# Kernel optimization log

Measured on AMD Instinct MI355X. Metric: run time of the kernel, lower is better.

Reference implementation:

```python
import jax, jax.numpy as jnp
import numpy as np

B, N, DM = 4, 4096, 768
H, LH = 12, 4          # total heads, local heads
GH = H - LH            # global (FAVOR+) heads
DH = DM // H           # 64, head dim
M = 256                # nb random features
W = 128                # local window size
EPS = 1e-4


def _gaussian_orthogonal_matrix(m, d, rng):
    # performer-pytorch gaussian_orthogonal_random_matrix, scaling=0
    blocks = []
    for _ in range(int(np.ceil(m / d))):
        q, _ = np.linalg.qr(rng.standard_normal((d, d)))
        blocks.append(q.T)
    mat = np.concatenate(blocks, 0)[:m]
    multiplier = np.linalg.norm(rng.standard_normal((m, d)), axis=-1)
    return (multiplier[:, None] * mat).astype(np.float32)


def setup_inputs() -> dict:
    key = jax.random.key(0)
    ks = jax.random.split(key, 6)
    s = 0.02
    x = jax.random.normal(ks[0], (B, N, DM), jnp.float32)
    mask = jnp.ones((B, N), dtype=bool)
    Wq = jax.random.normal(ks[1], (DM, DM), jnp.float32) * s
    Wk = jax.random.normal(ks[2], (DM, DM), jnp.float32) * s
    Wv = jax.random.normal(ks[3], (DM, DM), jnp.float32) * s
    Wo = jax.random.normal(ks[4], (DM, DM), jnp.float32) * s
    bo = jnp.zeros((DM,), jnp.float32)
    proj = jnp.asarray(_gaussian_orthogonal_matrix(M, DH, np.random.default_rng(0)))
    return {"x": x, "mask": mask, "Wq": Wq, "Wk": Wk, "Wv": Wv,
            "Wo": Wo, "bo": bo, "proj": proj}


def _softmax_kernel(data, proj, is_query):
    # FAVOR+ positive random features for the softmax kernel
    d = data.shape[-1]
    normalizer = d ** -0.25
    ratio = proj.shape[0] ** -0.5
    dd = jnp.einsum('bhnd,md->bhnm', data * normalizer, proj)
    diag = jnp.sum(data ** 2, axis=-1) * 0.5 * (normalizer ** 2)  # (b,h,n)
    if is_query:
        stab = jnp.max(dd, axis=-1, keepdims=True)
        return ratio * (jnp.exp(dd - diag[..., None] - stab) + EPS)
    stab = jnp.max(dd)
    return ratio * (jnp.exp(dd - diag[..., None] - stab) + EPS)


def _favor_attention(q, k, v, proj):
    # non-causal linear attention: O(n * m * d)
    qp = _softmax_kernel(q, proj, True)    # (b,gh,n,m)
    kp = _softmax_kernel(k, proj, False)   # (b,gh,n,m)
    k_sum = kp.sum(axis=2)                               # (b,gh,m)
    d_inv = 1.0 / jnp.einsum('bhnm,bhm->bhn', qp, k_sum)
    context = jnp.einsum('bhnm,bhnd->bhmd', kp, v)       # (b,gh,m,d)
    return jnp.einsum('bhmd,bhnm,bhn->bhnd', context, qp, d_inv)


def _rotary(x):
    # SinusoidalEmbeddings + apply_rotary_pos_emb (NeoX half-rotation)
    n, d = x.shape[-2], x.shape[-1]
    half = d // 2
    inv_freq = 1.0 / (10000.0 ** (jnp.arange(0, d, 2, dtype=jnp.float32) / d))
    freqs = jnp.arange(n, dtype=jnp.float32)[:, None] * inv_freq[None, :]
    emb = jnp.concatenate([freqs, freqs], axis=-1)       # (n,d)
    cos, sin = jnp.cos(emb), jnp.sin(emb)
    x1, x2 = x[..., :half], x[..., half:]
    rot = jnp.concatenate([-x2, x1], axis=-1)
    return x * cos + rot * sin


def _local_attention(lq, lk, lv, mask):
    # windowed attention, look_backward=1, look_forward=1 (non-causal)
    b, h, n, d = lq.shape
    lq, lk = _rotary(lq), _rotary(lk)
    nw = n // W
    bq = lq.reshape(b, h, nw, W, d)
    bk = lk.reshape(b, h, nw, W, d)
    bv = lv.reshape(b, h, nw, W, d)

    def look5(t):  # gather previous/current/next window along window axis
        p = jnp.pad(t, ((0, 0), (0, 0), (1, 1), (0, 0), (0, 0)))
        return jnp.concatenate([p[:, :, i:i + nw] for i in range(3)], axis=3)

    bk, bv = look5(bk), look5(bv)                        # (b,h,nw,3W,d)
    dots = jnp.einsum('bhwie,bhwje->bhwij', bq, bk) * (d ** -0.5)

    ticker = jnp.arange(n).reshape(nw, W)
    tp = jnp.pad(ticker, ((1, 1), (0, 0)), constant_values=-1)
    bq_k = jnp.concatenate([tp[i:i + nw] for i in range(3)], axis=1)  # (nw,3W)
    pad_ok = (bq_k != -1)[None, None, :, None, :]

    mq = mask.reshape(b, nw, W)
    mkp = jnp.pad(mq, ((0, 0), (1, 1), (0, 0)), constant_values=False)
    mk = jnp.concatenate([mkp[:, i:i + nw] for i in range(3)], axis=2)  # (b,nw,3W)
    inp_ok = (mq[:, :, :, None] & mk[:, :, None, :])[:, None]          # (b,1,nw,W,3W)

    neg = -jnp.finfo(dots.dtype).max
    dots = jnp.where(pad_ok & inp_ok, dots, neg)
    attn = jax.nn.softmax(dots, axis=-1)
    out = jnp.einsum('bhwij,bhwje->bhwie', attn, bv)
    return out.reshape(b, h, n, d)


def reference(x, mask, Wq, Wk, Wv, Wo, bo, proj):
    b, n, _ = x.shape
    split = lambda t: t.reshape(b, n, H, DH).transpose(0, 2, 1, 3)  # (b,h,n,d)
    q, k, v = split(x @ Wq), split(x @ Wk), split(x @ Wv)
    qg, lq = q[:, :GH], q[:, GH:]
    kg, lk = k[:, :GH], k[:, GH:]
    vg, lv = v[:, :GH], v[:, GH:]
    # global heads: zero masked values, FAVOR+ linear attention
    vg = jnp.where(mask[:, None, :, None], vg, 0.0)
    out_g = _favor_attention(qg, kg, vg, proj)
    out_l = _local_attention(lq, lk, lv, mask)
    out = jnp.concatenate([out_g, out_l], axis=1)        # (b,H,n,d)
    out = out.transpose(0, 2, 1, 3).reshape(b, n, DM)
    return out @ Wo + bo
```

## Files before the change

kernel.cpp:

```cpp
#include <hip/hip_runtime.h>
#include <hip/hip_fp16.h>
#include <math.h>

#define BB 4
#define NN 4096
#define DMM 768
#define HHH 12
#define LHH 4
#define GHH 8
#define DH 64
#define MM 256
#define WW 128
#define NWIN (NN/WW)
#define EPSF 1.0e-4f
#define NRM 0.35355339059327373f
#define NRM2 0.125f
#define RATIO 0.0625f
#define LN1E4_32 0.28782313662425572f

using bf16x8 = __attribute__((ext_vector_type(8))) short;
using fp16x8 = __attribute__((ext_vector_type(8))) _Float16;
using f32x4  = __attribute__((ext_vector_type(4))) float;

static __device__ __forceinline__ unsigned enc_f32(float f) {
  unsigned u = __float_as_uint(f);
  return (u & 0x80000000u) ? ~u : (u | 0x80000000u);
}
static __device__ __forceinline__ float dec_f32(unsigned u) {
  unsigned b = (u & 0x80000000u) ? (u ^ 0x80000000u) : ~u;
  return __uint_as_float(b);
}
static __device__ __forceinline__ unsigned short f2h(float x) {
  return __half_as_ushort(__float2half(x));
}
static __device__ __forceinline__ void gload16(const unsigned short* g, unsigned short* l) {
  __builtin_amdgcn_global_load_lds(
      (const __attribute__((address_space(1))) void*)g,
      (__attribute__((address_space(3))) void*)l, 16, 0, 0);
}

__global__ __launch_bounds__(256) void w_split(
    const float* __restrict__ W, unsigned short* __restrict__ Whi)
{
  int o = blockIdx.x * 256 + threadIdx.x;
  int k = o / DMM, n = o % DMM;
  Whi[(size_t)n * DMM + k] = f2h(W[o]);
}

__global__ __launch_bounds__(256) void a_split(
    const float* __restrict__ A, unsigned short* __restrict__ Ahi,
    unsigned short* __restrict__ Alo)
{
  size_t o = ((size_t)blockIdx.x * 256 + threadIdx.x) * 4;
  float4 v = *(const float4*)(A + o);
  float f[4] = {v.x, v.y, v.z, v.w};
  unsigned short hi[4], lo[4];
#pragma unroll
  for (int i = 0; i < 4; ++i) {
    __half h = __float2half(f[i]);
    hi[i] = __half_as_ushort(h);
    lo[i] = f2h(f[i] - __half2float(h));
  }
  *(uint2*)(Ahi + o) = *(uint2*)&hi[0];
  *(uint2*)(Alo + o) = *(uint2*)&lo[0];
}

__global__ __launch_bounds__(256) void gemm_mfma(
    const float* __restrict__ A, const unsigned short* __restrict__ Bhi,
    const float* __restrict__ bias, float* __restrict__ C, int K, int Nc)
{
  __shared__ unsigned short Ah[128][40];
  __shared__ unsigned short Al[128][40];
  __shared__ unsigned short Bh[128][40];

  const int tid = threadIdx.x;
  const int wid = tid >> 6, lane = tid & 63;
  const int quad = lane >> 4, l16 = lane & 15;
  const int row0 = blockIdx.y * 128;
  const int col0 = blockIdx.x * 128;
  const int wm = (wid & 1) * 64, wn = (wid >> 1) * 64;
  const int sr = tid >> 1;
  const int sk = (tid & 1) * 16;

  f32x4 acc[4][4];
  const f32x4 zf = {0.f, 0.f, 0.f, 0.f};
#pragma unroll
  for (int i = 0; i < 4; ++i)
#pragma unroll
    for (int j = 0; j < 4; ++j) acc[i][j] = zf;

  for (int k0 = 0; k0 < K; k0 += 32) {
    __syncthreads();
    {
      const float* a = A + (size_t)(row0 + sr) * K + k0 + sk;
      float fv[16];
      *(float4*)&fv[0]  = *(const float4*)(a);
      *(float4*)&fv[4]  = *(const float4*)(a + 4);
      *(float4*)&fv[8]  = *(const float4*)(a + 8);
      *(float4*)&fv[12] = *(const float4*)(a + 12);
      unsigned hw[8], lw[8];
#pragma unroll
      for (int p = 0; p < 8; ++p) {
        float x0 = fv[2 * p], x1 = fv[2 * p + 1];
        __half h0 = __float2half(x0), h1 = __float2half(x1);
        unsigned short l0 = f2h(x0 - __half2float(h0));
        unsigned short l1 = f2h(x1 - __half2float(h1));
        hw[p] = (unsigned)__half_as_ushort(h0) | ((unsigned)__half_as_ushort(h1) << 16);
        lw[p] = (unsigned)l0 | ((unsigned)l1 << 16);
      }
      *(uint4*)&Ah[sr][sk]     = *(uint4*)&hw[0];
      *(uint4*)&Ah[sr][sk + 8] = *(uint4*)&hw[4];
      *(uint4*)&Al[sr][sk]     = *(uint4*)&lw[0];
      *(uint4*)&Al[sr][sk + 8] = *(uint4*)&lw[4];
    }
    {
      const unsigned short* bh = Bhi + (size_t)(col0 + sr) * DMM + k0 + sk;
      *(uint4*)&Bh[sr][sk]     = *(const uint4*)(bh);
      *(uint4*)&Bh[sr][sk + 8] = *(const uint4*)(bh + 8);
    }
    __syncthreads();

    fp16x8 afh[4], afl[4], bfh[4];
#pragma unroll
    for (int t = 0; t < 4; ++t) {
      afh[t] = *(const fp16x8*)&Ah[wm + t * 16 + l16][quad * 8];
      afl[t] = *(const fp16x8*)&Al[wm + t * 16 + l16][quad * 8];
      bfh[t] = *(const fp16x8*)&Bh[wn + t * 16 + l16][quad * 8];
    }
#pragma unroll
    for (int ti = 0; ti < 4; ++ti)
#pragma unroll
      for (int tj = 0; tj < 4; ++tj) {
        acc[ti][tj] = __builtin_amdgcn_mfma_f32_16x16x32_f16(afh[ti], bfh[tj], acc[ti][tj], 0, 0, 0);
        acc[ti][tj] = __builtin_amdgcn_mfma_f32_16x16x32_f16(afl[ti], bfh[tj], acc[ti][tj], 0, 0, 0);
      }
  }

  float bv[4] = {0.f, 0.f, 0.f, 0.f};
  if (bias) {
#pragma unroll
    for (int tj = 0; tj < 4; ++tj) bv[tj] = bias[col0 + wn + tj * 16 + l16];
  }
#pragma unroll
  for (int ti = 0; ti < 4; ++ti) {
    const int gr = row0 + wm + ti * 16 + quad * 4;
#pragma unroll
    for (int tj = 0; tj < 4; ++tj) {
      const int gc = col0 + wn + tj * 16 + l16;
      float* cp = C + (size_t)gr * Nc + gc;
#pragma unroll
      for (int r = 0; r < 4; ++r)
        cp[(size_t)r * Nc] = acc[ti][tj][r] + bv[tj];
    }
  }
}

__global__ __launch_bounds__(256) void gemm_mfma_pre(
    const unsigned short* __restrict__ Ahi, const unsigned short* __restrict__ Alo,
    const unsigned short* __restrict__ Bhi,
    const float* __restrict__ bias, float* __restrict__ C, int K, int Nc)
{
  __shared__ unsigned short Ah[128][32];
  __shared__ unsigned short Al[128][32];
  __shared__ unsigned short Bh[128][32];

  const int tid = threadIdx.x;
  const int wid = tid >> 6, lane = tid & 63;
  const int quad = lane >> 4, l16 = lane & 15;

  const int nwg = gridDim.x * gridDim.y;
  int hw = blockIdx.y * gridDim.x + blockIdx.x;
  int logical = ((nwg & 7) == 0) ? ((hw & 7) * (nwg >> 3) + (hw >> 3)) : hw;
  const int col0 = (logical % gridDim.x) * 128;
  const int row0 = (logical / gridDim.x) * 128;

  const int wm = (wid & 1) * 64, wn = (wid >> 1) * 64;
  const int sw8 = (quad ^ ((l16 >> 1) & 3)) * 8;

  const int rr = tid >> 2;
  const int cg8 = ((tid & 3) ^ ((tid >> 3) & 3)) * 8;

  f32x4 acc[4][4];
  const f32x4 zf = {0.f, 0.f, 0.f, 0.f};
#pragma unroll
  for (int i = 0; i < 4; ++i)
#pragma unroll
    for (int j = 0; j < 4; ++j) acc[i][j] = zf;

  for (int k0 = 0; k0 < K; k0 += 32) {
    __syncthreads();
    {
      const size_t ro0 = (size_t)(row0 + rr) * K + k0 + cg8;
      const size_t ro1 = (size_t)(row0 + 64 + rr) * K + k0 + cg8;
      const size_t co0 = (size_t)(col0 + rr) * K + k0 + cg8;
      const size_t co1 = (size_t)(col0 + 64 + rr) * K + k0 + cg8;
      unsigned short* la  = &Ah[0][0] + tid * 8;
      unsigned short* lal = &Al[0][0] + tid * 8;
      unsigned short* lb  = &Bh[0][0] + tid * 8;
      gload16(Ahi + ro0, la);
      gload16(Ahi + ro1, la + 2048);
      gload16(Alo + ro0, lal);
      gload16(Alo + ro1, lal + 2048);
      gload16(Bhi + co0, lb);
      gload16(Bhi + co1, lb + 2048);
    }
    __syncthreads();

    fp16x8 afh[4], afl[4], bfh[4];
#pragma unroll
    for (int t = 0; t < 4; ++t) {
      afh[t] = *(const fp16x8*)&Ah[wm + t * 16 + l16][sw8];
      afl[t] = *(const fp16x8*)&Al[wm + t * 16 + l16][sw8];
      bfh[t] = *(const fp16x8*)&Bh[wn + t * 16 + l16][sw8];
    }
#pragma unroll
    for (int ti = 0; ti < 4; ++ti)
#pragma unroll
      for (int tj = 0; tj < 4; ++tj) {
        acc[ti][tj] = __builtin_amdgcn_mfma_f32_16x16x32_f16(afh[ti], bfh[tj], acc[ti][tj], 0, 0, 0);
        acc[ti][tj] = __builtin_amdgcn_mfma_f32_16x16x32_f16(afl[ti], bfh[tj], acc[ti][tj], 0, 0, 0);
      }
  }

  float bv[4] = {0.f, 0.f, 0.f, 0.f};
  if (bias) {
#pragma unroll
    for (int tj = 0; tj < 4; ++tj) bv[tj] = bias[col0 + wn + tj * 16 + l16];
  }
#pragma unroll
  for (int ti = 0; ti < 4; ++ti) {
    const int gr = row0 + wm + ti * 16 + quad * 4;
#pragma unroll
    for (int tj = 0; tj < 4; ++tj) {
      const int gc = col0 + wn + tj * 16 + l16;
      float* cp = C + (size_t)gr * Nc + gc;
#pragma unroll
      for (int r = 0; r < 4; ++r)
        cp[(size_t)r * Nc] = acc[ti][tj][r] + bv[tj];
    }
  }
}

__global__ void init_stab(unsigned* stab_enc) {
  if (threadIdx.x == 0 && blockIdx.x == 0) *stab_enc = 0x00800000u;
}

__global__ __launch_bounds__(256) void transpose_proj(
    const float* __restrict__ proj, float* __restrict__ projT,
    unsigned short* __restrict__ phh, unsigned short* __restrict__ phl)
{
  int o = blockIdx.x * 256 + threadIdx.x;
  int k = o >> 8, m = o & 255;
  float v = proj[m * 64 + k];
  projT[k * 256 + m] = v;
  __half hh = __float2half(v);
  float lf = v - __half2float(hh);
  phh[m * 64 + k] = __half_as_ushort(hh);
  phl[m * 64 + k] = f2h(lf);
}

__global__ __launch_bounds__(256) void rot_qk(
    const float* __restrict__ Qb, const float* __restrict__ Kb,
    unsigned short* __restrict__ Qlh, unsigned short* __restrict__ Klh)
{
  int idx = blockIdx.x * 256 + threadIdx.x;
  int n = idx & (NN - 1);
  int bh = idx >> 12;
  int b = bh >> 2, h = bh & 3;
  const float* qs = Qb + ((size_t)(b * NN + n)) * DMM + GHH * DH + h * DH;
  const float* ks = Kb + ((size_t)(b * NN + n)) * DMM + GHH * DH + h * DH;
  float q[64], k[64];
#pragma unroll
  for (int t = 0; t < 16; ++t) {
    *(float4*)&q[t * 4] = *(const float4*)(qs + t * 4);
    *(float4*)&k[t * 4] = *(const float4*)(ks + t * 4);
  }
  unsigned short qo[64], ko[64];
#pragma unroll
  for (int i = 0; i < 32; ++i) {
    float invf = __expf((float)i * -LN1E4_32);
    float th = (float)n * invf;
    float s, c;
    sincosf(th, &s, &c);
    qo[i]      = f2h(fmaf(q[i], c, -q[i + 32] * s) * NRM2);
    qo[i + 32] = f2h(fmaf(q[i + 32], c, q[i] * s) * NRM2);
    ko[i]      = f2h(fmaf(k[i], c, -k[i + 32] * s));
    ko[i + 32] = f2h(fmaf(k[i + 32], c, k[i] * s));
  }
  unsigned short* qd = Qlh + (size_t)idx * 64;
  unsigned short* kd = Klh + (size_t)idx * 64;
#pragma unroll
  for (int t = 0; t < 8; ++t) {
    *(uint4*)(qd + t * 8) = *(uint4*)&qo[t * 8];
    *(uint4*)(kd + t * 8) = *(uint4*)&ko[t * 8];
  }
}

__global__ __launch_bounds__(256) void v_trans(
    const float* __restrict__ Vb, unsigned short* __restrict__ Vt)
{
  __shared__ unsigned short T[64][72];
  const int nb = blockIdx.x, h = blockIdx.y, b = blockIdx.z;
  const int n0 = nb * 64;
  const int tid = threadIdx.x;
  {
    int r = tid >> 2, g = tid & 3;
    const float* src = Vb + ((size_t)(b * NN + n0 + r)) * DMM + GHH * DH + h * DH + g * 16;
#pragma unroll
    for (int t = 0; t < 4; ++t) {
      float4 v = *(const float4*)(src + t * 4);
      T[g * 16 + t * 4 + 0][r] = f2h(v.x);
      T[g * 16 + t * 4 + 1][r] = f2h(v.y);
      T[g * 16 + t * 4 + 2][r] = f2h(v.z);
      T[g * 16 + t * 4 + 3][r] = f2h(v.w);
    }
  }
  __syncthreads();
  {
    int d = tid >> 2, g = tid & 3;
    unsigned short* dst = Vt + ((size_t)(b * LHH + h) * DH + d) * NN + n0 + g * 16;
    *(uint4*)dst       = *(uint4*)&T[d][g * 16];
    *(uint4*)(dst + 8) = *(uint4*)&T[d][g * 16 + 8];
  }
}

__global__ __launch_bounds__(256) void local_attn2(
    const unsigned short* __restrict__ Qlh, const unsigned short* __restrict__ Klh,
    const unsigned short* __restrict__ Vt, float* __restrict__ Qb)
{
  __shared__ unsigned short Pl[4][32][72];
  const int w = blockIdx.x, h = blockIdx.y, b = blockIdx.z;
  const int tid = threadIdx.x;
  const int wid = tid >> 6, lane = tid & 63;
  const int quad = lane >> 4, l16 = lane & 15;
  const int bh = b * LHH + h;
  const int qn0 = w * WW + wid * 32;

  fp16x8 Aq[2][2];
#pragma unroll
  for (int mt = 0; mt < 2; ++mt)
#pragma unroll
    for (int ks = 0; ks < 2; ++ks)
      Aq[mt][ks] = *(const fp16x8*)(Qlh + ((size_t)bh * NN + qn0 + mt * 16 + l16) * 64 + ks * 32 + quad * 8);

  float m_run[8], l_run[8];
  f32x4 Oacc[2][4];
  const f32x4 zf = {0.f, 0.f, 0.f, 0.f};
#pragma unroll
  for (int r = 0; r < 8; ++r) { m_run[r] = -3.4e38f; l_run[r] = 0.f; }
#pragma unroll
  for (int mt = 0; mt < 2; ++mt)
#pragma unroll
    for (int nt = 0; nt < 4; ++nt) Oacc[mt][nt] = zf;

  const int wb_lo = (w == 0) ? 0 : w - 1;
  const int wb_hi = (w == NWIN - 1) ? w : w + 1;
  for (int wb = wb_lo; wb <= wb_hi; ++wb) {
    for (int half = 0; half < 2; ++half) {
      const int kn0 = wb * WW + half * 64;
      f32x4 sacc[2][4];
#pragma unroll
      for (int mt = 0; mt < 2; ++mt)
#pragma unroll
        for (int nt = 0; nt < 4; ++nt) sacc[mt][nt] = zf;

#pragma unroll
      for (int ks = 0; ks < 2; ++ks) {
        fp16x8 Bk[4];
#pragma unroll
        for (int nt = 0; nt < 4; ++nt)
          Bk[nt] = *(const fp16x8*)(Klh + ((size_t)bh * NN + kn0 + nt * 16 + l16) * 64 + ks * 32 + quad * 8);
#pragma unroll
        for (int mt = 0; mt < 2; ++mt)
#pragma unroll
          for (int nt = 0; nt < 4; ++nt)
            sacc[mt][nt] = __builtin_amdgcn_mfma_f32_16x16x32_f16(Aq[mt][ks], Bk[nt], sacc[mt][nt], 0, 0, 0);
      }

#pragma unroll
      for (int mt = 0; mt < 2; ++mt) {
#pragma unroll
        for (int reg = 0; reg < 4; ++reg) {
          const int r8 = mt * 4 + reg;
          float v = fmaxf(fmaxf(sacc[mt][0][reg], sacc[mt][1][reg]),
                          fmaxf(sacc[mt][2][reg], sacc[mt][3][reg]));
          v = fmaxf(v, __shfl_xor(v, 1));
          v = fmaxf(v, __shfl_xor(v, 2));
          v = fmaxf(v, __shfl_xor(v, 4));
          v = fmaxf(v, __shfl_xor(v, 8));
          float mnew = fmaxf(m_run[r8], v);
          float alpha = __expf(m_run[r8] - mnew);
          m_run[r8] = mnew;
          float ps = 0.f;
#pragma unroll
          for (int nt = 0; nt < 4; ++nt) {
            float p = __expf(sacc[mt][nt][reg] - mnew);
            sacc[mt][nt][reg] = p;
            ps += p;
          }
          ps += __shfl_xor(ps, 1);
          ps += __shfl_xor(ps, 2);
          ps += __shfl_xor(ps, 4);
          ps += __shfl_xor(ps, 8);
          l_run[r8] = l_run[r8] * alpha + ps;
#pragma unroll
          for (int nt = 0; nt < 4; ++nt) Oacc[mt][nt][reg] *= alpha;
        }
      }

#pragma unroll
      for (int mt = 0; mt < 2; ++mt)
#pragma unroll
        for (int nt = 0; nt < 4; ++nt)
#pragma unroll
          for (int reg = 0; reg < 4; ++reg)
            Pl[wid][mt * 16 + quad * 4 + reg][nt * 16 + l16] = f2h(sacc[mt][nt][reg]);

#pragma unroll
      for (int kstep = 0; kstep < 2; ++kstep) {
        fp16x8 Ap[2];
#pragma unroll
        for (int mt = 0; mt < 2; ++mt)
          Ap[mt] = *(const fp16x8*)&Pl[wid][mt * 16 + l16][kstep * 32 + quad * 8];
        fp16x8 Bv[4];
#pragma unroll
        for (int nt = 0; nt < 4; ++nt)
          Bv[nt] = *(const fp16x8*)(Vt + ((size_t)bh * DH + nt * 16 + l16) * NN + kn0 + kstep * 32 + quad * 8);
#pragma unroll
        for (int mt = 0; mt < 2; ++mt)
#pragma unroll
          for (int nt = 0; nt < 4; ++nt)
            Oacc[mt][nt] = __builtin_amdgcn_mfma_f32_16x16x32_f16(Ap[mt], Bv[nt], Oacc[mt][nt], 0, 0, 0);
      }
    }
  }

#pragma unroll
  for (int mt = 0; mt < 2; ++mt)
#pragma unroll
    for (int reg = 0; reg < 4; ++reg) {
      const float inv = 1.0f / l_run[mt * 4 + reg];
      const int n = qn0 + mt * 16 + quad * 4 + reg;
      float* dst = Qb + ((size_t)(b * NN + n)) * DMM + GHH * DH + h * DH;
#pragma unroll
      for (int nt = 0; nt < 4; ++nt)
        dst[nt * 16 + l16] = Oacc[mt][nt][reg] * inv;
    }
}

__global__ __launch_bounds__(256) void favor_kstab_mfma(
    const float* __restrict__ Kg, const unsigned short* __restrict__ phh,
    const unsigned short* __restrict__ phl, unsigned* __restrict__ stab_enc)
{
  __shared__ unsigned short Khh[64][72];
  __shared__ unsigned short Khl[64][72];
  __shared__ float wred[4];
  const int tid = threadIdx.x;
  const int wid = tid >> 6, lane = tid & 63;
  const int quad = lane >> 4, l16 = lane & 15;
  const int chunk = blockIdx.x & 63;
  const int bh = blockIdx.x >> 6;
  const int b = bh >> 3, h = bh & 7;
  const int n0 = chunk * 64;
  const f32x4 zf = {0.f, 0.f, 0.f, 0.f};

  {
    const int r = tid >> 2, s2 = tid & 3;
    const float* ksrc = Kg + ((size_t)(b * NN + n0 + r)) * DMM + h * DH + s2 * 16;
    unsigned short th[16], tl[16];
#pragma unroll
    for (int t = 0; t < 4; ++t) {
      float4 g = *(const float4*)(ksrc + t * 4);
      float f[4] = {g.x * NRM, g.y * NRM, g.z * NRM, g.w * NRM};
#pragma unroll
      for (int j = 0; j < 4; ++j) {
        __half hh = __float2half(f[j]);
        th[t * 4 + j] = __half_as_ushort(hh);
        tl[t * 4 + j] = f2h(f[j] - __half2float(hh));
      }
    }
    *(uint4*)&Khh[r][s2 * 16]     = *(uint4*)&th[0];
    *(uint4*)&Khh[r][s2 * 16 + 8] = *(uint4*)&th[8];
    *(uint4*)&Khl[r][s2 * 16]     = *(uint4*)&tl[0];
    *(uint4*)&Khl[r][s2 * 16 + 8] = *(uint4*)&tl[8];
  }
  __syncthreads();

  const int wn0 = wid * 64;
  f32x4 acc[4][4];
#pragma unroll
  for (int i = 0; i < 4; ++i)
#pragma unroll
    for (int j = 0; j < 4; ++j) acc[i][j] = zf;

#pragma unroll
  for (int ks = 0; ks < 2; ++ks) {
    fp16x8 afh[4], afl[4], bfh[4], bfl[4];
#pragma unroll
    for (int t = 0; t < 4; ++t) {
      afh[t] = *(const fp16x8*)&Khh[t * 16 + l16][ks * 32 + quad * 8];
      afl[t] = *(const fp16x8*)&Khl[t * 16 + l16][ks * 32 + quad * 8];
      const size_t po = (size_t)(wn0 + t * 16 + l16) * 64 + ks * 32 + quad * 8;
      bfh[t] = *(const fp16x8*)(phh + po);
      bfl[t] = *(const fp16x8*)(phl + po);
    }
#pragma unroll
    for (int mt = 0; mt < 4; ++mt)
#pragma unroll
      for (int nt = 0; nt < 4; ++nt) {
        acc[mt][nt] = __builtin_amdgcn_mfma_f32_16x16x32_f16(afh[mt], bfh[nt], acc[mt][nt], 0, 0, 0);
        acc[mt][nt] = __builtin_amdgcn_mfma_f32_16x16x32_f16(afh[mt], bfl[nt], acc[mt][nt], 0, 0, 0);
        acc[mt][nt] = __builtin_amdgcn_mfma_f32_16x16x32_f16(afl[mt], bfh[nt], acc[mt][nt], 0, 0, 0);
      }
  }

  float mx = -3.4e38f;
#pragma unroll
  for (int mt = 0; mt < 4; ++mt)
#pragma unroll
    for (int nt = 0; nt < 4; ++nt)
#pragma unroll
      for (int r = 0; r < 4; ++r) mx = fmaxf(mx, acc[mt][nt][r]);
#pragma unroll
  for (int off = 32; off; off >>= 1) mx = fmaxf(mx, __shfl_xor(mx, off));
  if (lane == 0) wred[wid] = mx;
  __syncthreads();
  if (tid == 0) {
    float m2 = fmaxf(fmaxf(wred[0], wred[1]), fmaxf(wred[2], wred[3]));
    atomicMax(stab_enc, enc_f32(m2));
  }
}

__global__ __launch_bounds__(256, 2) void favor_ctx_mfma(
    const float* __restrict__ Kg, const float* __restrict__ Vg,
    const unsigned short* __restrict__ phh, const unsigned short* __restrict__ phl,
    const unsigned* __restrict__ stab_enc,
    float* __restrict__ ctxp, float* __restrict__ ksump, int split)
{
  __shared__ unsigned short Khh[64][72];
  __shared__ unsigned short Khl[64][72];
  __shared__ unsigned short Vt_h[64][72];
  __shared__ unsigned short kp_s[256][72];
  __shared__ float diag_s[64];

  const int tid = threadIdx.x;
  const int wid = tid >> 6, lane = tid & 63;
  const int quad = lane >> 4, l16 = lane & 15;
  const int sidx = blockIdx.x % split;
  const int bh = blockIdx.x / split;
  const int b = bh >> 3, h = bh & 7;
  const int rows = NN / split, nch = rows / 64;
  const float stab = dec_f32(*stab_enc);
  const int wn0 = wid * 64;
  const f32x4 zf = {0.f, 0.f, 0.f, 0.f};

  f32x4 acc2[4][4];
#pragma unroll
  for (int i = 0; i < 4; ++i)
#pragma unroll
    for (int j = 0; j < 4; ++j) acc2[i][j] = zf;
  float ksacc[4] = {0.f, 0.f, 0.f, 0.f};

  for (int c = 0; c < nch; ++c) {
    const int n0 = sidx * rows + c * 64;
    __syncthreads();
    {
      const int r = tid >> 2, s2 = tid & 3;
      const float* ksrc = Kg + ((size_t)(b * NN + n0 + r)) * DMM + h * DH + s2 * 16;
      const float* vsrc = Vg + ((size_t)(b * NN + n0 + r)) * DMM + h * DH + s2 * 16;
      float kq = 0.f;
      unsigned short th[16], tl[16];
#pragma unroll
      for (int t = 0; t < 4; ++t) {
        float4 g = *(const float4*)(ksrc + t * 4);
        float f[4] = {g.x * NRM, g.y * NRM, g.z * NRM, g.w * NRM};
#pragma unroll
        for (int j = 0; j < 4; ++j) {
          kq = fmaf(f[j], f[j], kq);
          __half hh = __float2half(f[j]);
          th[t * 4 + j] = __half_as_ushort(hh);
          tl[t * 4 + j] = f2h(f[j] - __half2float(hh));
        }
        float4 vv = *(const float4*)(vsrc + t * 4);
        Vt_h[s2 * 16 + t * 4 + 0][r] = f2h(vv.x);
        Vt_h[s2 * 16 + t * 4 + 1][r] = f2h(vv.y);
        Vt_h[s2 * 16 + t * 4 + 2][r] = f2h(vv.z);
        Vt_h[s2 * 16 + t * 4 + 3][r] = f2h(vv.w);
      }
      *(uint4*)&Khh[r][s2 * 16]     = *(uint4*)&th[0];
      *(uint4*)&Khh[r][s2 * 16 + 8] = *(uint4*)&th[8];
      *(uint4*)&Khl[r][s2 * 16]     = *(uint4*)&tl[0];
      *(uint4*)&Khl[r][s2 * 16 + 8] = *(uint4*)&tl[8];
      kq += __shfl_xor(kq, 1);
      kq += __shfl_xor(kq, 2);
      if (s2 == 0) diag_s[r] = 0.5f * kq;
    }
    __syncthreads();

    f32x4 acc[4][4];
#pragma unroll
    for (int i = 0; i < 4; ++i)
#pragma unroll
      for (int j = 0; j < 4; ++j) acc[i][j] = zf;
#pragma unroll
    for (int ks = 0; ks < 2; ++ks) {
      fp16x8 afh[4], afl[4], bfh[4], bfl[4];
#pragma unroll
      for (int t = 0; t < 4; ++t) {
        afh[t] = *(const fp16x8*)&Khh[t * 16 + l16][ks * 32 + quad * 8];
        afl[t] = *(const fp16x8*)&Khl[t * 16 + l16][ks * 32 + quad * 8];
        const size_t po = (size_t)(wn0 + t * 16 + l16) * 64 + ks * 32 + quad * 8;
        bfh[t] = *(const fp16x8*)(phh + po);
        bfl[t] = *(const fp16x8*)(phl + po);
      }
#pragma unroll
      for (int mt = 0; mt < 4; ++mt)
#pragma unroll
        for (int nt = 0; nt < 4; ++nt) {
          acc[mt][nt] = __builtin_amdgcn_mfma_f32_16x16x32_f16(afh[mt], bfh[nt], acc[mt][nt], 0, 0, 0);
          acc[mt][nt] = __builtin_amdgcn_mfma_f32_16x16x32_f16(afh[mt], bfl[nt], acc[mt][nt], 0, 0, 0);
          acc[mt][nt] = __builtin_amdgcn_mfma_f32_16x16x32_f16(afl[mt], bfh[nt], acc[mt][nt], 0, 0, 0);
        }
    }

    float ks_i[4] = {0.f, 0.f, 0.f, 0.f};
#pragma unroll
    for (int mt = 0; mt < 4; ++mt) {
#pragma unroll
      for (int nt = 0; nt < 4; ++nt) {
        float pv[4];
#pragma unroll
        for (int reg = 0; reg < 4; ++reg) {
          const int n = mt * 16 + quad * 4 + reg;
          float p = RATIO * (__expf(acc[mt][nt][reg] - diag_s[n] - stab) + EPSF);
          pv[reg] = p;
          ks_i[nt] += p;
        }
        __half2 h0 = __floats2half2_rn(pv[0], pv[1]);
        __half2 h1 = __floats2half2_rn(pv[2], pv[3]);
        uint2 w;
        w.x = *(unsigned*)&h0;
        w.y = *(unsigned*)&h1;
        *(uint2*)&kp_s[wn0 + nt * 16 + l16][mt * 16 + quad * 4] = w;
      }
    }
#pragma unroll
    for (int nt = 0; nt < 4; ++nt) {
      float s = ks_i[nt];
      s += __shfl_xor(s, 16);
      s += __shfl_xor(s, 32);
      ksacc[nt] += s;
    }
    __syncthreads();

#pragma unroll
    for (int ks2 = 0; ks2 < 2; ++ks2) {
      fp16x8 ap[4], bv[4];
#pragma unroll
      for (int t = 0; t < 4; ++t) {
        ap[t] = *(const fp16x8*)&kp_s[wn0 + t * 16 + l16][ks2 * 32 + quad * 8];
        bv[t] = *(const fp16x8*)&Vt_h[t * 16 + l16][ks2 * 32 + quad * 8];
      }
#pragma unroll
      for (int mt = 0; mt < 4; ++mt)
#pragma unroll
        for (int nt = 0; nt < 4; ++nt)
          acc2[mt][nt] = __builtin_amdgcn_mfma_f32_16x16x32_f16(ap[mt], bv[nt], acc2[mt][nt], 0, 0, 0);
    }
  }

  {
    float* dst = ctxp + ((size_t)(bh * split + sidx)) * MM * DH;
#pragma unroll
    for (int mt = 0; mt < 4; ++mt)
#pragma unroll
      for (int nt = 0; nt < 4; ++nt) {
        const int m = wn0 + mt * 16 + quad * 4;
        const int d = nt * 16 + l16;
        *(f32x4*)(dst + (size_t)d * MM + m) = acc2[mt][nt];
      }
    if (quad == 0) {
      float* kd = ksump + (size_t)(bh * split + sidx) * MM;
#pragma unroll
      for (int nt = 0; nt < 4; ++nt) kd[wn0 + nt * 16 + l16] = ksacc[nt];
    }
  }
}

__global__ __launch_bounds__(256) void favor_reduce(
    const float* __restrict__ ctxp, const float* __restrict__ ksump,
    unsigned short* __restrict__ ctxT_h, float* __restrict__ ksum, int split)
{
  int i = blockIdx.x * 256 + threadIdx.x;
  if (i < BB * GHH * MM * DH) {
    int bh = i / (MM * DH);
    int md = i % (MM * DH);
    float s = 0.f;
    for (int k = 0; k < split; ++k) s += ctxp[((size_t)(bh * split + k)) * MM * DH + md];
    ctxT_h[i] = f2h(s);
  }
  if (i < BB * GHH * MM) {
    int bh = i / MM, m = i % MM;
    float s = 0.f;
    for (int k = 0; k < split; ++k) s += ksump[(bh * split + k) * MM + m];
    ksum[i] = s;
  }
}

__global__ __launch_bounds__(256, 2) void favor_out_mfma(
    float* __restrict__ Q, const unsigned short* __restrict__ phh,
    const unsigned short* __restrict__ phl,
    const unsigned short* __restrict__ ctxT_h, const float* __restrict__ ksum)
{
  __shared__ unsigned short Qhh[64][72];
  __shared__ unsigned short Qhl[64][72];
  __shared__ unsigned short qp_s[64][264];
  __shared__ float red[4][64];
  __shared__ float dred[4][64];
  __shared__ float diag4[64][4];
  __shared__ float diag_s[64];
  __shared__ float dinv_s[64];
  __shared__ float ksum_s[256];

  const int tid = threadIdx.x;
  const int wid = tid >> 6, lane = tid & 63;
  const int quad = lane >> 4, l16 = lane & 15;
  const int bh = blockIdx.x >> 6;
  const int chunk = blockIdx.x & 63;
  const int b = bh >> 3, h = bh & 7;
  const int n0 = chunk * 64;
  const f32x4 zf = {0.f, 0.f, 0.f, 0.f};

  {
    const int r = tid >> 2, s2 = tid & 3;
    const float* src = Q + ((size_t)(b * NN + n0 + r)) * DMM + h * DH + s2 * 16;
    float sq = 0.f;
    unsigned short th[16], tl[16];
#pragma unroll
    for (int t = 0; t < 4; ++t) {
      float4 g = *(const float4*)(src + t * 4);
      float f[4] = {g.x * NRM, g.y * NRM, g.z * NRM, g.w * NRM};
#pragma unroll
      for (int j = 0; j < 4; ++j) {
        sq = fmaf(f[j], f[j], sq);
        __half hh = __float2half(f[j]);
        th[t * 4 + j] = __half_as_ushort(hh);
        tl[t * 4 + j] = f2h(f[j] - __half2float(hh));
      }
    }
    diag4[r][s2] = sq;
    *(uint4*)&Qhh[r][s2 * 16]     = *(uint4*)&th[0];
    *(uint4*)&Qhh[r][s2 * 16 + 8] = *(uint4*)&th[8];
    *(uint4*)&Qhl[r][s2 * 16]     = *(uint4*)&tl[0];
    *(uint4*)&Qhl[r][s2 * 16 + 8] = *(uint4*)&tl[8];
    ksum_s[tid] = ksum[bh * MM + tid];
  }
  __syncthreads();
  if (tid < 64)
    diag_s[tid] = 0.5f * (diag4[tid][0] + diag4[tid][1] + diag4[tid][2] + diag4[tid][3]);

  const int wn0 = wid * 64;
  f32x4 acc[4][4];
#pragma unroll
  for (int i = 0; i < 4; ++i)
#pragma unroll
    for (int j = 0; j < 4; ++j) acc[i][j] = zf;

#pragma unroll
  for (int ks = 0; ks < 2; ++ks) {
    fp16x8 afh[4], afl[4], bfh[4], bfl[4];
#pragma unroll
    for (int t = 0; t < 4; ++t) {
      afh[t] = *(const fp16x8*)&Qhh[t * 16 + l16][ks * 32 + quad * 8];
      afl[t] = *(const fp16x8*)&Qhl[t * 16 + l16][ks * 32 + quad * 8];
      const size_t po = (size_t)(wn0 + t * 16 + l16) * 64 + ks * 32 + quad * 8;
      bfh[t] = *(const fp16x8*)(phh + po);
      bfl[t] = *(const fp16x8*)(phl + po);
    }
#pragma unroll
    for (int mt = 0; mt < 4; ++mt)
#pragma unroll
      for (int nt = 0; nt < 4; ++nt) {
        acc[mt][nt] = __builtin_amdgcn_mfma_f32_16x16x32_f16(afh[mt], bfh[nt], acc[mt][nt], 0, 0, 0);
        acc[mt][nt] = __builtin_amdgcn_mfma_f32_16x16x32_f16(afh[mt], bfl[nt], acc[mt][nt], 0, 0, 0);
        acc[mt][nt] = __builtin_amdgcn_mfma_f32_16x16x32_f16(afl[mt], bfh[nt], acc[mt][nt], 0, 0, 0);
      }
  }

#pragma unroll
  for (int mt = 0; mt < 4; ++mt)
#pragma unroll
    for (int reg = 0; reg < 4; ++reg) {
      float v = fmaxf(fmaxf(acc[mt][0][reg], acc[mt][1][reg]),
                      fmaxf(acc[mt][2][reg], acc[mt][3][reg]));
      v = fmaxf(v, __shfl_xor(v, 1));
      v = fmaxf(v, __shfl_xor(v, 2));
      v = fmaxf(v, __shfl_xor(v, 4));
      v = fmaxf(v, __shfl_xor(v, 8));
      if (l16 == 0) red[wid][mt * 16 + quad * 4 + reg] = v;
    }
  __syncthreads();

  float ksv[4];
#pragma unroll
  for (int nt = 0; nt < 4; ++nt) ksv[nt] = ksum_s[wn0 + nt * 16 + l16];
#pragma unroll
  for (int mt = 0; mt < 4; ++mt)
#pragma unroll
    for (int reg = 0; reg < 4; ++reg) {
      const int row = mt * 16 + quad * 4 + reg;
      float stab = fmaxf(fmaxf(red[0][row], red[1][row]),
                         fmaxf(red[2][row], red[3][row]));
      float base = diag_s[row] + stab;
      float dsum = 0.f;
#pragma unroll
      for (int nt = 0; nt < 4; ++nt) {
        float p = RATIO * (__expf(acc[mt][nt][reg] - base) + EPSF);
        acc[mt][nt][reg] = p;
        dsum = fmaf(p, ksv[nt], dsum);
      }
      dsum += __shfl_xor(dsum, 1);
      dsum += __shfl_xor(dsum, 2);
      dsum += __shfl_xor(dsum, 4);
      dsum += __shfl_xor(dsum, 8);
      if (l16 == 0) dred[wid][row] = dsum;
#pragma unroll
      for (int nt = 0; nt < 4; ++nt)
        qp_s[row][wn0 + nt * 16 + l16] = f2h(acc[mt][nt][reg]);
    }
  __syncthreads();
  if (tid < 64)
    dinv_s[tid] = 1.0f / (dred[0][tid] + dred[1][tid] + dred[2][tid] + dred[3][tid]);

  const int wn2 = wid * 16;
  f32x4 acc2[4];
#pragma unroll
  for (int mt = 0; mt < 4; ++mt) acc2[mt] = zf;
#pragma unroll
  for (int ksp = 0; ksp < 8; ++ksp) {
    fp16x8 bv = *(const fp16x8*)(ctxT_h + ((size_t)bh * DH + wn2 + l16) * MM + ksp * 32 + quad * 8);
    fp16x8 ap[4];
#pragma unroll
    for (int mt = 0; mt < 4; ++mt)
      ap[mt] = *(const fp16x8*)&qp_s[mt * 16 + l16][ksp * 32 + quad * 8];
#pragma unroll
    for (int mt = 0; mt < 4; ++mt)
      acc2[mt] = __builtin_amdgcn_mfma_f32_16x16x32_f16(ap[mt], bv, acc2[mt], 0, 0, 0);
  }
  __syncthreads();

#pragma unroll
  for (int mt = 0; mt < 4; ++mt)
#pragma unroll
    for (int reg = 0; reg < 4; ++reg) {
      const int row = mt * 16 + quad * 4 + reg;
      Q[((size_t)(b * NN + n0 + row)) * DMM + h * DH + wn2 + l16] =
          acc2[mt][reg] * dinv_s[row];
    }
}

extern "C" void kernel_launch(void* const* d_in, const int* in_sizes, int n_in,
                              void* d_out, int out_size, void* d_ws, size_t ws_size,
                              hipStream_t stream)
{
  (void)in_sizes; (void)n_in; (void)out_size;
  const float* x    = (const float*)d_in[0];
  const float* Wq   = (const float*)d_in[2];
  const float* Wk   = (const float*)d_in[3];
  const float* Wv   = (const float*)d_in[4];
  const float* Wo   = (const float*)d_in[5];
  const float* bo   = (const float*)d_in[6];
  const float* proj = (const float*)d_in[7];
  float* out = (float*)d_out;

  const size_t WSZ = (size_t)DMM * DMM;
  const size_t XSP = (size_t)BB * NN * DMM;
  const size_t wbuf_f = (8 * WSZ * 2 + 3) / 4;
  const size_t LSZ = (size_t)BB * LHH * NN * DH;
  const size_t lbuf_f = (3 * LSZ * 2 + 3) / 4;
  const size_t fixed_f = (size_t)3 * XSP + (size_t)BB * GHH * MM * DH
                       + (size_t)BB * GHH * MM + 16 + MM * DH + MM * DH + 16
                       + wbuf_f + 16 + lbuf_f + 16;

  int split = 8, use_pre = 0;
  for (int s = 32; s >= 8; s >>= 1) {
    size_t part = (size_t)BB * GHH * s * (MM * DH + MM);
    size_t region = part > XSP ? part : XSP;
    if ((fixed_f + region) * 4 <= ws_size) { split = s; use_pre = 1; break; }
  }
  if (!use_pre) {
    for (int s = 32; s >= 8; s >>= 1) {
      size_t need = (fixed_f + (size_t)BB * GHH * s * (MM * DH + MM)) * 4;
      if (need <= ws_size) { split = s; break; }
    }
  }
  size_t part_f = (size_t)BB * GHH * split * (MM * DH + MM);
  size_t region_f = (use_pre && XSP > part_f) ? XSP : part_f;

  float* Qb    = (float*)d_ws;
  float* Kb    = Qb + XSP;
  float* Vb    = Kb + XSP;
  float* region = Vb + XSP;
  float* ctxp  = region;
  float* ksump = ctxp + (size_t)BB * GHH * split * MM * DH;
  unsigned short* xH = (unsigned short*)region;
  unsigned short* xL = xH + XSP;
  float* ctx   = region + region_f;
  unsigned short* ctxT_h = (unsigned short*)ctx;
  float* ksum  = ctx + (size_t)BB * GHH * MM * DH;
  unsigned* stab = (unsigned*)(ksum + BB * GHH * MM);
  float* projT = (float*)(stab + 16);
  unsigned short* proj_hh = (unsigned short*)(projT + MM * DH);
  unsigned short* proj_hl = proj_hh + MM * DH;
  unsigned short* wsp = proj_hl + MM * DH;
  unsigned short* WqH = wsp;
  unsigned short* WkH = wsp + 2 * WSZ;
  unsigned short* WvH = wsp + 4 * WSZ;
  unsigned short* WoH = wsp + 6 * WSZ;
  unsigned short* Qlh = wsp + 8 * WSZ;
  unsigned short* Klh = Qlh + LSZ;
  unsigned short* Vtl = Klh + LSZ;

  dim3 blk(256);
  dim3 mg(DMM / 128, (BB * NN) / 128);
  const int wgrid = (int)(WSZ / 256);
  const int agrid = (int)(XSP / 1024);

  w_split<<<wgrid, blk, 0, stream>>>(Wq, WqH);
  w_split<<<wgrid, blk, 0, stream>>>(Wk, WkH);
  w_split<<<wgrid, blk, 0, stream>>>(Wv, WvH);
  w_split<<<wgrid, blk, 0, stream>>>(Wo, WoH);
  if (use_pre) {
    a_split<<<agrid, blk, 0, stream>>>(x, xH, xL);
    gemm_mfma_pre<<<mg, blk, 0, stream>>>(xH, xL, WqH, nullptr, Qb, DMM, DMM);
    gemm_mfma_pre<<<mg, blk, 0, stream>>>(xH, xL, WkH, nullptr, Kb, DMM, DMM);
    gemm_mfma_pre<<<mg, blk, 0, stream>>>(xH, xL, WvH, nullptr, Vb, DMM, DMM);
  } else {
    gemm_mfma<<<mg, blk, 0, stream>>>(x, WqH, nullptr, Qb, DMM, DMM);
    gemm_mfma<<<mg, blk, 0, stream>>>(x, WkH, nullptr, Kb, DMM, DMM);
    gemm_mfma<<<mg, blk, 0, stream>>>(x, WvH, nullptr, Vb, DMM, DMM);
  }
  rot_qk<<<(BB * LHH * NN) / 256, blk, 0, stream>>>(Qb, Kb, Qlh, Klh);
  v_trans<<<dim3(NN / 64, LHH, BB), blk, 0, stream>>>(Vb, Vtl);
  init_stab<<<1, 64, 0, stream>>>(stab);
  transpose_proj<<<64, blk, 0, stream>>>(proj, projT, proj_hh, proj_hl);
  favor_kstab_mfma<<<BB * GHH * (NN / 64), blk, 0, stream>>>(Kb, proj_hh, proj_hl, stab);
  favor_ctx_mfma<<<BB * GHH * split, blk, 0, stream>>>(Kb, Vb, proj_hh, proj_hl, stab, ctxp, ksump, split);
  favor_reduce<<<(BB * GHH * MM * DH) / 256, blk, 0, stream>>>(ctxp, ksump, ctxT_h, ksum, split);
  favor_out_mfma<<<BB * GHH * (NN / 64), blk, 0, stream>>>(Qb, proj_hh, proj_hl, ctxT_h, ksum);
  local_attn2<<<dim3(NWIN, LHH, BB), blk, 0, stream>>>(Qlh, Klh, Vtl, Qb);
  if (use_pre) {
    a_split<<<agrid, blk, 0, stream>>>(Qb, xH, xL);
    gemm_mfma_pre<<<mg, blk, 0, stream>>>(xH, xL, WoH, bo, out, DMM, DMM);
  } else {
    gemm_mfma<<<mg, blk, 0, stream>>>(Qb, WoH, bo, out, DMM, DMM);
  }
}
```

Baseline: 546.4 us.

## Fuse QKV projections into one GEMM and emit split-fp16 attention outputs directly

The three Q/K/V projection GEMMs become one launch over a 3x-wide grid, with the epilogue routing each column tile to its own output buffer. The FAVOR output and local attention kernels now write the hi/lo fp16 split of their results straight into the buffers the output-projection GEMM reads. This removes the separate a_split pass over the attention output. favor_out_mfma drops its LDS staging of Q and the diag/dinv shared arrays, computing the squared norm in registers with shuffles, and loses its occupancy hint. The unused fp32 projT copy is removed, and the weight buffer shrinks since the fused layout reuses space.

```diff
diff --git a/kernel.cpp b/kernel.cpp
--- a/kernel.cpp
+++ b/kernel.cpp
@@ -18,7 +18,6 @@
 #define RATIO 0.0625f
 #define LN1E4_32 0.28782313662425572f
 
-using bf16x8 = __attribute__((ext_vector_type(8))) short;
 using fp16x8 = __attribute__((ext_vector_type(8))) _Float16;
 using f32x4  = __attribute__((ext_vector_type(4))) float;
 
@@ -158,7 +157,8 @@
 __global__ __launch_bounds__(256) void gemm_mfma_pre(
     const unsigned short* __restrict__ Ahi, const unsigned short* __restrict__ Alo,
     const unsigned short* __restrict__ Bhi,
-    const float* __restrict__ bias, float* __restrict__ C, int K, int Nc)
+    const float* __restrict__ bias, float* __restrict__ C, int K,
+    int colsPerBuf, size_t bufStride)
 {
   __shared__ unsigned short Ah[128][32];
   __shared__ unsigned short Al[128][32];
@@ -222,6 +222,10 @@
       }
   }
 
+  const int buf = col0 / colsPerBuf;
+  const int cc0 = col0 % colsPerBuf;
+  float* Cb = C + (size_t)buf * bufStride;
+
   float bv[4] = {0.f, 0.f, 0.f, 0.f};
   if (bias) {
 #pragma unroll
@@ -232,11 +236,11 @@
     const int gr = row0 + wm + ti * 16 + quad * 4;
 #pragma unroll
     for (int tj = 0; tj < 4; ++tj) {
-      const int gc = col0 + wn + tj * 16 + l16;
-      float* cp = C + (size_t)gr * Nc + gc;
+      const int gc = cc0 + wn + tj * 16 + l16;
+      float* cp = Cb + (size_t)gr * colsPerBuf + gc;
 #pragma unroll
       for (int r = 0; r < 4; ++r)
-        cp[(size_t)r * Nc] = acc[ti][tj][r] + bv[tj];
+        cp[(size_t)r * colsPerBuf] = acc[ti][tj][r] + bv[tj];
     }
   }
 }
@@ -246,13 +250,12 @@
 }
 
 __global__ __launch_bounds__(256) void transpose_proj(
-    const float* __restrict__ proj, float* __restrict__ projT,
+    const float* __restrict__ proj,
     unsigned short* __restrict__ phh, unsigned short* __restrict__ phl)
 {
   int o = blockIdx.x * 256 + threadIdx.x;
   int k = o >> 8, m = o & 255;
   float v = proj[m * 64 + k];
-  projT[k * 256 + m] = v;
   __half hh = __float2half(v);
   float lf = v - __half2float(hh);
   phh[m * 64 + k] = __half_as_ushort(hh);
@@ -326,7 +329,8 @@
 
 __global__ __launch_bounds__(256) void local_attn2(
     const unsigned short* __restrict__ Qlh, const unsigned short* __restrict__ Klh,
-    const unsigned short* __restrict__ Vt, float* __restrict__ Qb)
+    const unsigned short* __restrict__ Vt, float* __restrict__ Qb,
+    unsigned short* __restrict__ xH, unsigned short* __restrict__ xL, int split_out)
 {
   __shared__ unsigned short Pl[4][32][72];
   const int w = blockIdx.x, h = blockIdx.y, b = blockIdx.z;
@@ -441,10 +445,20 @@
     for (int reg = 0; reg < 4; ++reg) {
       const float inv = 1.0f / l_run[mt * 4 + reg];
       const int n = qn0 + mt * 16 + quad * 4 + reg;
-      float* dst = Qb + ((size_t)(b * NN + n)) * DMM + GHH * DH + h * DH;
-#pragma unroll
-      for (int nt = 0; nt < 4; ++nt)
-        dst[nt * 16 + l16] = Oacc[mt][nt][reg] * inv;
+      const size_t base = ((size_t)(b * NN + n)) * DMM + GHH * DH + h * DH;
+      if (split_out) {
+#pragma unroll
+        for (int nt = 0; nt < 4; ++nt) {
+          float o = Oacc[mt][nt][reg] * inv;
+          __half hh = __float2half(o);
+          xH[base + nt * 16 + l16] = __half_as_ushort(hh);
+          xL[base + nt * 16 + l16] = f2h(o - __half2float(hh));
+        }
+      } else {
+#pragma unroll
+        for (int nt = 0; nt < 4; ++nt)
+          Qb[base + nt * 16 + l16] = Oacc[mt][nt][reg] * inv;
+      }
     }
 }
 
@@ -707,20 +721,15 @@
   }
 }
 
-__global__ __launch_bounds__(256, 2) void favor_out_mfma(
+__global__ __launch_bounds__(256) void favor_out_mfma(
     float* __restrict__ Q, const unsigned short* __restrict__ phh,
     const unsigned short* __restrict__ phl,
-    const unsigned short* __restrict__ ctxT_h, const float* __restrict__ ksum)
-{
-  __shared__ unsigned short Qhh[64][72];
-  __shared__ unsigned short Qhl[64][72];
+    const unsigned short* __restrict__ ctxT_h, const float* __restrict__ ksum,
+    unsigned short* __restrict__ xH, unsigned short* __restrict__ xL, int split_out)
+{
   __shared__ unsigned short qp_s[64][264];
   __shared__ float red[4][64];
   __shared__ float dred[4][64];
-  __shared__ float diag4[64][4];
-  __shared__ float diag_s[64];
-  __shared__ float dinv_s[64];
-  __shared__ float ksum_s[256];
 
   const int tid = threadIdx.x;
   const int wid = tid >> 6, lane = tid & 63;
@@ -729,50 +738,40 @@
   const int chunk = blockIdx.x & 63;
   const int b = bh >> 3, h = bh & 7;
   const int n0 = chunk * 64;
+  const int wn0 = wid * 64;
   const f32x4 zf = {0.f, 0.f, 0.f, 0.f};
 
-  {
-    const int r = tid >> 2, s2 = tid & 3;
-    const float* src = Q + ((size_t)(b * NN + n0 + r)) * DMM + h * DH + s2 * 16;
-    float sq = 0.f;
-    unsigned short th[16], tl[16];
-#pragma unroll
-    for (int t = 0; t < 4; ++t) {
-      float4 g = *(const float4*)(src + t * 4);
-      float f[4] = {g.x * NRM, g.y * NRM, g.z * NRM, g.w * NRM};
-#pragma unroll
-      for (int j = 0; j < 4; ++j) {
-        sq = fmaf(f[j], f[j], sq);
-        __half hh = __float2half(f[j]);
-        th[t * 4 + j] = __half_as_ushort(hh);
-        tl[t * 4 + j] = f2h(f[j] - __half2float(hh));
-      }
-    }
-    diag4[r][s2] = sq;
-    *(uint4*)&Qhh[r][s2 * 16]     = *(uint4*)&th[0];
-    *(uint4*)&Qhh[r][s2 * 16 + 8] = *(uint4*)&th[8];
-    *(uint4*)&Qhl[r][s2 * 16]     = *(uint4*)&tl[0];
-    *(uint4*)&Qhl[r][s2 * 16 + 8] = *(uint4*)&tl[8];
-    ksum_s[tid] = ksum[bh * MM + tid];
-  }
-  __syncthreads();
-  if (tid < 64)
-    diag_s[tid] = 0.5f * (diag4[tid][0] + diag4[tid][1] + diag4[tid][2] + diag4[tid][3]);
-
-  const int wn0 = wid * 64;
+  float ksv[4];
+#pragma unroll
+  for (int nt = 0; nt < 4; ++nt) ksv[nt] = ksum[bh * MM + wn0 + nt * 16 + l16];
+
   f32x4 acc[4][4];
 #pragma unroll
   for (int i = 0; i < 4; ++i)
 #pragma unroll
     for (int j = 0; j < 4; ++j) acc[i][j] = zf;
+  float dsq[4] = {0.f, 0.f, 0.f, 0.f};
 
 #pragma unroll
   for (int ks = 0; ks < 2; ++ks) {
     fp16x8 afh[4], afl[4], bfh[4], bfl[4];
 #pragma unroll
     for (int t = 0; t < 4; ++t) {
-      afh[t] = *(const fp16x8*)&Qhh[t * 16 + l16][ks * 32 + quad * 8];
-      afl[t] = *(const fp16x8*)&Qhl[t * 16 + l16][ks * 32 + quad * 8];
+      const float* src = Q + ((size_t)(b * NN + n0 + t * 16 + l16)) * DMM + h * DH + ks * 32 + quad * 8;
+      float f[8];
+      *(float4*)&f[0] = *(const float4*)src;
+      *(float4*)&f[4] = *(const float4*)(src + 4);
+      unsigned short th[8], tl[8];
+#pragma unroll
+      for (int j = 0; j < 8; ++j) {
+        float v = f[j] * NRM;
+        dsq[t] = fmaf(v, v, dsq[t]);
+        __half hh = __float2half(v);
+        th[j] = __half_as_ushort(hh);
+        tl[j] = f2h(v - __half2float(hh));
+      }
+      afh[t] = *(const fp16x8*)&th[0];
+      afl[t] = *(const fp16x8*)&tl[0];
       const size_t po = (size_t)(wn0 + t * 16 + l16) * 64 + ks * 32 + quad * 8;
       bfh[t] = *(const fp16x8*)(phh + po);
       bfl[t] = *(const fp16x8*)(phl + po);
@@ -785,6 +784,11 @@
         acc[mt][nt] = __builtin_amdgcn_mfma_f32_16x16x32_f16(afh[mt], bfl[nt], acc[mt][nt], 0, 0, 0);
         acc[mt][nt] = __builtin_amdgcn_mfma_f32_16x16x32_f16(afl[mt], bfh[nt], acc[mt][nt], 0, 0, 0);
       }
+  }
+#pragma unroll
+  for (int t = 0; t < 4; ++t) {
+    dsq[t] += __shfl_xor(dsq[t], 16);
+    dsq[t] += __shfl_xor(dsq[t], 32);
   }
 
 #pragma unroll
@@ -801,17 +805,15 @@
     }
   __syncthreads();
 
-  float ksv[4];
-#pragma unroll
-  for (int nt = 0; nt < 4; ++nt) ksv[nt] = ksum_s[wn0 + nt * 16 + l16];
 #pragma unroll
   for (int mt = 0; mt < 4; ++mt)
 #pragma unroll
     for (int reg = 0; reg < 4; ++reg) {
       const int row = mt * 16 + quad * 4 + reg;
+      float dq = __shfl(dsq[mt], quad * 4 + reg);
       float stab = fmaxf(fmaxf(red[0][row], red[1][row]),
                          fmaxf(red[2][row], red[3][row]));
-      float base = diag_s[row] + stab;
+      float base = 0.5f * dq + stab;
       float dsum = 0.f;
 #pragma unroll
       for (int nt = 0; nt < 4; ++nt) {
@@ -829,8 +831,6 @@
         qp_s[row][wn0 + nt * 16 + l16] = f2h(acc[mt][nt][reg]);
     }
   __syncthreads();
-  if (tid < 64)
-    dinv_s[tid] = 1.0f / (dred[0][tid] + dred[1][tid] + dred[2][tid] + dred[3][tid]);
 
   const int wn2 = wid * 16;
   f32x4 acc2[4];
@@ -847,15 +847,22 @@
     for (int mt = 0; mt < 4; ++mt)
       acc2[mt] = __builtin_amdgcn_mfma_f32_16x16x32_f16(ap[mt], bv, acc2[mt], 0, 0, 0);
   }
-  __syncthreads();
 
 #pragma unroll
   for (int mt = 0; mt < 4; ++mt)
 #pragma unroll
     for (int reg = 0; reg < 4; ++reg) {
       const int row = mt * 16 + quad * 4 + reg;
-      Q[((size_t)(b * NN + n0 + row)) * DMM + h * DH + wn2 + l16] =
-          acc2[mt][reg] * dinv_s[row];
+      float ds = dred[0][row] + dred[1][row] + dred[2][row] + dred[3][row];
+      float o = acc2[mt][reg] / ds;
+      const size_t base = ((size_t)(b * NN + n0 + row)) * DMM + h * DH + wn2 + l16;
+      if (split_out) {
+        __half hh = __float2half(o);
+        xH[base] = __half_as_ushort(hh);
+        xL[base] = f2h(o - __half2float(hh));
+      } else {
+        Q[base] = o;
+      }
     }
 }
 
@@ -875,11 +882,11 @@
 
   const size_t WSZ = (size_t)DMM * DMM;
   const size_t XSP = (size_t)BB * NN * DMM;
-  const size_t wbuf_f = (8 * WSZ * 2 + 3) / 4;
+  const size_t wbuf_f = (4 * WSZ * 2 + 3) / 4;
   const size_t LSZ = (size_t)BB * LHH * NN * DH;
   const size_t lbuf_f = (3 * LSZ * 2 + 3) / 4;
   const size_t fixed_f = (size_t)3 * XSP + (size_t)BB * GHH * MM * DH
-                       + (size_t)BB * GHH * MM + 16 + MM * DH + MM * DH + 16
+                       + (size_t)BB * GHH * MM + 16 + MM * DH + 16
                        + wbuf_f + 16 + lbuf_f + 16;
 
   int split = 8, use_pre = 0;
@@ -909,50 +916,45 @@
   unsigned short* ctxT_h = (unsigned short*)ctx;
   float* ksum  = ctx + (size_t)BB * GHH * MM * DH;
   unsigned* stab = (unsigned*)(ksum + BB * GHH * MM);
-  float* projT = (float*)(stab + 16);
-  unsigned short* proj_hh = (unsigned short*)(projT + MM * DH);
+  unsigned short* proj_hh = (unsigned short*)(stab + 16);
   unsigned short* proj_hl = proj_hh + MM * DH;
   unsigned short* wsp = proj_hl + MM * DH;
-  unsigned short* WqH = wsp;
-  unsigned short* WkH = wsp + 2 * WSZ;
-  unsigned short* WvH = wsp + 4 * WSZ;
-  unsigned short* WoH = wsp + 6 * WSZ;
-  unsigned short* Qlh = wsp + 8 * WSZ;
+  unsigned short* WqkvH = wsp;
+  unsigned short* WoH   = wsp + 3 * WSZ;
+  unsigned short* Qlh = wsp + 4 * WSZ;
   unsigned short* Klh = Qlh + LSZ;
   unsigned short* Vtl = Klh + LSZ;
 
   dim3 blk(256);
-  dim3 mg(DMM / 128, (BB * NN) / 128);
+  dim3 mgq(3 * DMM / 128, (BB * NN) / 128);
+  dim3 mgo(DMM / 128, (BB * NN) / 128);
   const int wgrid = (int)(WSZ / 256);
   const int agrid = (int)(XSP / 1024);
 
-  w_split<<<wgrid, blk, 0, stream>>>(Wq, WqH);
-  w_split<<<wgrid, blk, 0, stream>>>(Wk, WkH);
-  w_split<<<wgrid, blk, 0, stream>>>(Wv, WvH);
+  w_split<<<wgrid, blk, 0, stream>>>(Wq, WqkvH);
+  w_split<<<wgrid, blk, 0, stream>>>(Wk, WqkvH + WSZ);
+  w_split<<<wgrid, blk, 0, stream>>>(Wv, WqkvH + 2 * WSZ);
   w_split<<<wgrid, blk, 0, stream>>>(Wo, WoH);
   if (use_pre) {
     a_split<<<agrid, blk, 0, stream>>>(x, xH, xL);
-    gemm_mfma_pre<<<mg, blk, 0, stream>>>(xH, xL, WqH, nullptr, Qb, DMM, DMM);
-    gemm_mfma_pre<<<mg, blk, 0, stream>>>(xH, xL, WkH, nullptr, Kb, DMM, DMM);
-    gemm_mfma_pre<<<mg, blk, 0, stream>>>(xH, xL, WvH, nullptr, Vb, DMM, DMM);
+    gemm_mfma_pre<<<mgq, blk, 0, stream>>>(xH, xL, WqkvH, nullptr, Qb, DMM, DMM, XSP);
   } else {
-    gemm_mfma<<<mg, blk, 0, stream>>>(x, WqH, nullptr, Qb, DMM, DMM);
-    gemm_mfma<<<mg, blk, 0, stream>>>(x, WkH, nullptr, Kb, DMM, DMM);
-    gemm_mfma<<<mg, blk, 0, stream>>>(x, WvH, nullptr, Vb, DMM, DMM);
+    gemm_mfma<<<mgo, blk, 0, stream>>>(x, WqkvH, nullptr, Qb, DMM, DMM);
+    gemm_mfma<<<mgo, blk, 0, stream>>>(x, WqkvH + WSZ, nullptr, Kb, DMM, DMM);
+    gemm_mfma<<<mgo, blk, 0, stream>>>(x, WqkvH + 2 * WSZ, nullptr, Vb, DMM, DMM);
   }
   rot_qk<<<(BB * LHH * NN) / 256, blk, 0, stream>>>(Qb, Kb, Qlh, Klh);
   v_trans<<<dim3(NN / 64, LHH, BB), blk, 0, stream>>>(Vb, Vtl);
   init_stab<<<1, 64, 0, stream>>>(stab);
-  transpose_proj<<<64, blk, 0, stream>>>(proj, projT, proj_hh, proj_hl);
+  transpose_proj<<<64, blk, 0, stream>>>(proj, proj_hh, proj_hl);
   favor_kstab_mfma<<<BB * GHH * (NN / 64), blk, 0, stream>>>(Kb, proj_hh, proj_hl, stab);
   favor_ctx_mfma<<<BB * GHH * split, blk, 0, stream>>>(Kb, Vb, proj_hh, proj_hl, stab, ctxp, ksump, split);
   favor_reduce<<<(BB * GHH * MM * DH) / 256, blk, 0, stream>>>(ctxp, ksump, ctxT_h, ksum, split);
-  favor_out_mfma<<<BB * GHH * (NN / 64), blk, 0, stream>>>(Qb, proj_hh, proj_hl, ctxT_h, ksum);
-  local_attn2<<<dim3(NWIN, LHH, BB), blk, 0, stream>>>(Qlh, Klh, Vtl, Qb);
+  favor_out_mfma<<<BB * GHH * (NN / 64), blk, 0, stream>>>(Qb, proj_hh, proj_hl, ctxT_h, ksum, xH, xL, use_pre);
+  local_attn2<<<dim3(NWIN, LHH, BB), blk, 0, stream>>>(Qlh, Klh, Vtl, Qb, xH, xL, use_pre);
   if (use_pre) {
-    a_split<<<agrid, blk, 0, stream>>>(Qb, xH, xL);
-    gemm_mfma_pre<<<mg, blk, 0, stream>>>(xH, xL, WoH, bo, out, DMM, DMM);
+    gemm_mfma_pre<<<mgo, blk, 0, stream>>>(xH, xL, WoH, bo, out, DMM, DMM, 0);
   } else {
-    gemm_mfma<<<mg, blk, 0, stream>>>(Qb, WoH, bo, out, DMM, DMM);
-  }
-}
+    gemm_mfma<<<mgo, blk, 0, stream>>>(Qb, WoH, bo, out, DMM, DMM);
+  }
+}
```

Measured after the change: 593.0 us. 1.09x slower.
